# Optimization experiments

Measured on AMD Instinct MI355X. Metric: run time of the kernel, lower is better.

## Reference

```python
import jax, jax.numpy as jnp
import numpy as np

B, N = 32, 512


def _stick_breaking(b, x_mask):
    """Row-major stick-breaking recurrence, O(N^2) sequential steps.

    Equivalent to the TF while_loop: for step in range(N*N), m=step//N, n=step%N:
      fut      = max(0, x_mask[:,m,n+1:] - sum_{m'<m} x[:,m',n+1:])  (col partial sums)
      mfm      = sum_j fut_j
      row_sum  = sum_{n'<n} x[:,m,n']
      col_sum  = sum_{m'<m} x[:,m',n]
      lower    = mask[m,n]*max(0, 1 - row_sum - mfm)
      upper    = mask[m,n]*min(1 - row_sum, 1 - col_sum)
      x[m,n]   = lower + b[m,n]*(upper - lower)
    Key insight: during row m the column partial sums are constant, so the
    future-mass terms for every n can be precomputed as an exclusive reverse
    cumsum; only the within-row dependency (row_sum) needs a scan.
    """
    Bb, Nn, _ = b.shape
    dt = b.dtype

    def row_step(col_sums, inputs):
        b_row, mask_row = inputs                      # [B, N] each
        fut = jnp.maximum(0.0, mask_row - col_sums)   # [B, N]
        # mfm[:, n] = sum_{j > n} fut[:, j]  (exclusive reverse cumsum)
        mfm = jnp.flip(jnp.cumsum(jnp.flip(fut, -1), axis=-1), -1) - fut

        def col_step(row_sum, inp):
            b_mn, m_mn, mfm_n, cs_n = inp             # [B] each
            lower = m_mn * jnp.maximum(0.0, 1.0 - row_sum - mfm_n)
            upper = m_mn * jnp.minimum(1.0 - row_sum, 1.0 - cs_n)
            p = lower + b_mn * (upper - lower)
            return row_sum + p, p

        _, row = jax.lax.scan(
            col_step,
            jnp.zeros((Bb,), dt),
            (b_row.T, mask_row.T, mfm.T, col_sums.T),
        )
        row = row.T                                   # [B, N]
        return col_sums + row, row

    _, rows = jax.lax.scan(
        row_step,
        jnp.zeros((Bb, Nn), dt),
        (jnp.swapaxes(b, 0, 1), jnp.swapaxes(x_mask, 0, 1)),
    )
    return jnp.swapaxes(rows, 0, 1)                   # [B, N, N]


def setup_inputs() -> dict:
    key = jax.random.key(0)
    k1, _ = jax.random.split(key)
    x = jax.random.normal(k1, (B, N, N), dtype=jnp.float32)
    x_mask = jnp.ones((B, N, N), dtype=jnp.float32)
    return {"x": x, "x_mask": x_mask}


def reference(x, x_mask):
    # layer.call applies sigmoid to the logits before stick-breaking
    return _stick_breaking(jax.nn.sigmoid(x), x_mask)
```

## Files before the change

### kernel.cpp

```cpp
#include <hip/hip_runtime.h>

#define NBATCH 32
#define NDIM 512
#define NFAST 448
#define NPAIR 224
#define NWAVE 8


template <int CTRL, int RMASK>
__device__ __forceinline__ float dpp_add(float x) {
  int t = __builtin_amdgcn_update_dpp(0, __float_as_int(x), CTRL, RMASK, 0xf,
                                      false);
  return x + __int_as_float(t);
}

__device__ __forceinline__ float prefix_inc(float x) {
  x = dpp_add<0x111, 0xf>(x);
  x = dpp_add<0x112, 0xf>(x);
  x = dpp_add<0x114, 0xf>(x);
  x = dpp_add<0x118, 0xf>(x);
  x = dpp_add<0x142, 0xa>(x);
  x = dpp_add<0x143, 0xc>(x);
  return x;
}

__device__ __forceinline__ float wave_shr1(float x, float fill) {
  return __int_as_float(__builtin_amdgcn_update_dpp(
      __float_as_int(fill), __float_as_int(x), 0x138 , 0xf, 0xf,
      false));
}

template <int CTRL, int RMASK>
__device__ __forceinline__ void aff_step(float& A, float& B) {
  float Ae = __int_as_float(__builtin_amdgcn_update_dpp(
      __float_as_int(1.0f), __float_as_int(A), CTRL, RMASK, 0xf, false));
  float Be = __int_as_float(__builtin_amdgcn_update_dpp(
      0, __float_as_int(B), CTRL, RMASK, 0xf, false));
  B = fmaf(A, Be, B);
  A = A * Ae;
}

__device__ __forceinline__ void wg_barrier() {
  asm volatile("s_waitcnt lgkmcnt(0)" ::: "memory");
  __builtin_amdgcn_s_barrier();
  asm volatile("" ::: "memory");
}

__global__ __launch_bounds__(512, 2)
void sb_kernel(const float* __restrict__ x, const float* __restrict__ xm,
               float* __restrict__ out) {
  const int tid = (int)threadIdx.x;
  const int lane = tid & 63;
  const int w = __builtin_amdgcn_readfirstlane(tid >> 6);
  const size_t base =
      (size_t)blockIdx.x * NDIM * NDIM + (size_t)(w * 64 + lane);
  const float* xb = x + base;
  const float* mb = xm + base;
  float* ob = out + base;

  __shared__ float4 recs[NFAST];
  __shared__ alignas(16) float ex_sa[NWAVE];
  __shared__ alignas(16) float ex_S[NWAVE];
  __shared__ alignas(16) float ex_A[NWAVE];
  __shared__ alignas(16) float ex_B[NWAVE];

  float w8, t8;
  float c2_0, oc2_0, c2_1, oc2_1;
  float c1, c2, oc2;
  float fu = 0.0f, S = 0.0f;

  float X0 = xb[0], M0 = mb[0];
  float X1 = xb[NDIM], M1 = mb[NDIM];
  float p1x0 = xb[2 * NDIM], p1x1 = xb[3 * NDIM];
  float p1m0 = mb[2 * NDIM], p1m1 = mb[3 * NDIM];
  float p2x0 = xb[4 * NDIM], p2x1 = xb[5 * NDIM];
  float p2m0 = mb[4 * NDIM], p2m1 = mb[5 * NDIM];

  float Ax0, Ax1, Am0, Am1;
  float Bx0, Bx1, Bm0, Bm1;
  float Cx0, Cx1, Cm0, Cm1;
  Ax0 = Bx0 = Cx0 = p1x0;
  Ax1 = Bx1 = Cx1 = p1x1;
  Am0 = Bm0 = Cm0 = p1m0;
  Am1 = Bm1 = Cm1 = p1m1;
  switch (w % 3) {
    case 0:
      Bx0 = p1x0; Bx1 = p1x1; Bm0 = p1m0; Bm1 = p1m1;
      Cx0 = p2x0; Cx1 = p2x1; Cm0 = p2m0; Cm1 = p2m1;
      break;
    case 1:
      Cx0 = p1x0; Cx1 = p1x1; Cm0 = p1m0; Cm1 = p1m1;
      Ax0 = p2x0; Ax1 = p2x1; Am0 = p2m0; Am1 = p2m1;
      break;
    default:
      Ax0 = p1x0; Ax1 = p1x1; Am0 = p1m0; Am1 = p1m1;
      Bx0 = p2x0; Bx1 = p2x1; Bm0 = p2m0; Bm1 = p2m1;
      break;
  }

  {
    float sg0 = __builtin_amdgcn_rcpf(1.0f + __expf(-X0));
    c2_0 = M0 * sg0;
    oc2_0 = 1.0f - c2_0;
    float sg1 = __builtin_amdgcn_rcpf(1.0f + __expf(-X1));
    c2_1 = M1 * sg1;
    oc2_1 = 1.0f - c2_1;
    w8 = 1.0f;
    t8 = c2_0;
  }

  const float* px = xb + (long)(6 - 2 * w) * NDIM;
  const float* pm = mb + (long)(6 - 2 * w) * NDIM;
  float* po = ob - (long)(2 * w) * NDIM;

  auto row_fast = [&](int m, const float4& r, float c2r, float oc2r,
                      float* pO) {
    float PA = prefix_inc(t8);
    float uin = fmaxf(1.0f - (r.z + (PA - t8)), 0.0f);
    bool pW = w8 < uin;
    float A = pW ? 1.0f : oc2r;
    float Bv = pW ? (-t8) : 0.0f;
    aff_step<0x111, 0xf>(A, Bv);
    aff_step<0x112, 0xf>(A, Bv);
    aff_step<0x114, 0xf>(A, Bv);
    aff_step<0x118, 0xf>(A, Bv);
    aff_step<0x142, 0xa>(A, Bv);
    aff_step<0x143, 0xc>(A, Bv);
    float Aex = wave_shr1(A, 1.0f);
    float Bex = wave_shr1(Bv, 0.0f);
    if (w < NWAVE - 1 && lane == 63)
      recs[m] = make_float4(A * r.x, fmaf(A, r.y, Bv), r.z + PA, 0.0f);
    float E = r.x + r.y;
    float e = fminf(fmaxf(fmaf(Aex, E, Bex), 0.0f), 1.0f);
    float p = c2r * fminf(e, w8);
    w8 -= p;
    *pO = p;
  };

  auto pair_step = [&](int t, int k, float& WX0, float& WX1, float& WM0,
                       float& WM1, const float& RX0, const float& RX1,
                       const float& RM0, const float& RM1) {
    const int s = t - w;
    if ((unsigned)s < (unsigned)NPAIR) {
      const int m = 2 * s;
      float4 r0 = make_float4(1.0f, 0.0f, 0.0f, 0.0f), r1 = r0;
      if (w > 0) {
        r0 = recs[m];
        r1 = recs[m + 1];
      }
      const float* pxk = px + (size_t)(2 * k) * NDIM;
      const float* pmk = pm + (size_t)(2 * k) * NDIM;
      float LX0 = pxk[0], LX1 = pxk[NDIM];
      float LM0 = pmk[0], LM1 = pmk[NDIM];

      float sg0 = __builtin_amdgcn_rcpf(1.0f + __expf(-RX0));
      float c2n0 = RM0 * sg0;
      float oc2n0 = 1.0f - c2n0;
      float sg1 = __builtin_amdgcn_rcpf(1.0f + __expf(-RX1));
      float c2n1 = RM1 * sg1;
      float oc2n1 = 1.0f - c2n1;

      float* pok = po + (size_t)(2 * k) * NDIM;
      row_fast(m, r0, c2_0, oc2_0, pok);
      t8 = c2_1 * w8;
      row_fast(m + 1, r1, c2_1, oc2_1, pok + NDIM);
      t8 = c2n0 * w8;
      c2_0 = c2n0;
      oc2_0 = oc2n0;
      c2_1 = c2n1;
      oc2_1 = oc2n1;
      WX0 = LX0;
      WX1 = LX1;
      WM0 = LM0;
      WM1 = LM1;
    }
    wg_barrier();
  };

#pragma unroll 1
  for (int t = 0; t < NPAIR + NWAVE - 1; t += 3) {
    pair_step(t + 0, 0, Ax0, Ax1, Am0, Am1, Bx0, Bx1, Bm0, Bm1);
    pair_step(t + 1, 1, Bx0, Bx1, Bm0, Bm1, Cx0, Cx1, Cm0, Cm1);
    pair_step(t + 2, 2, Cx0, Cx1, Cm0, Cm1, Ax0, Ax1, Am0, Am1);
    px += 6 * NDIM;
    pm += 6 * NDIM;
    po += 6 * NDIM;
  }

  float fx0, fm0, fx1, fm1, fx2, fm2, fx3, fm3;
  {
    float m448 = mb[(size_t)448 * NDIM];
    fx1 = xb[(size_t)449 * NDIM];
    fm1 = mb[(size_t)449 * NDIM];
    fx2 = xb[(size_t)450 * NDIM];
    fm2 = mb[(size_t)450 * NDIM];
    fx3 = xb[(size_t)451 * NDIM];
    fm3 = mb[(size_t)451 * NDIM];
    fx0 = fx1;
    fm0 = fm1;
    c2 = c2_0;
    oc2 = oc2_0;
    c1 = m448 - c2;
    float om = 1.0f - m448;
    fu = fmaxf(w8 - om, 0.0f);
    S = fu;
  }

  auto row_full = [&](int m, float& WX, float& WM, const float& RX,
                      const float& RM) {
    const size_t nro = (size_t)((m + 4) & (NDIM - 1)) * NDIM;
    WX = xb[nro];
    WM = mb[nro];

    float PS = prefix_inc(S);
    float PA = prefix_inc(t8);

    if (lane == 63) {
      ex_sa[w] = PA;
      ex_S[w] = PS;
    }
    wg_barrier();

    float4 sl = *(const float4*)&ex_sa[0];
    float4 sh = *(const float4*)&ex_sa[4];
    float4 Sl = *(const float4*)&ex_S[0];
    float4 Sh = *(const float4*)&ex_S[4];
    float off_sa = 0.0f, off_S = 0.0f;
    if (w > 0) { off_sa += sl.x; off_S += Sl.x; }
    if (w > 1) { off_sa += sl.y; off_S += Sl.y; }
    if (w > 2) { off_sa += sl.z; off_S += Sl.z; }
    if (w > 3) { off_sa += sl.w; off_S += Sl.w; }
    if (w > 4) { off_sa += sh.x; off_S += Sh.x; }
    if (w > 5) { off_sa += sh.y; off_S += Sh.y; }
    if (w > 6) { off_sa += sh.z; off_S += Sh.z; }
    float Tg =
        ((Sl.x + Sl.y) + (Sl.z + Sl.w)) + ((Sh.x + Sh.y) + (Sh.z + Sh.w));

    float uin = fmaxf(1.0f - (off_sa + (PA - t8)), 0.0f);
    float R_ = (Tg - off_S) - PS;
    float nc1m = -c1 * R_;

    bool pW = w8 < uin;
    float aP = pW ? 1.0f : oc2;
    float bP = pW ? (-t8) : 0.0f;
    bool pL = (uin - R_) > 0.0f;
    if (pL) {
      aP -= c1;
      bP -= nc1m;
    }

    float A = aP, Bv = bP;
    aff_step<0x111, 0xf>(A, Bv);
    aff_step<0x112, 0xf>(A, Bv);
    aff_step<0x114, 0xf>(A, Bv);
    aff_step<0x118, 0xf>(A, Bv);
    aff_step<0x142, 0xa>(A, Bv);
    aff_step<0x143, 0xc>(A, Bv);
    float Aex = wave_shr1(A, 1.0f);
    float Bex = wave_shr1(Bv, 0.0f);

    if (lane == 63) {
      ex_A[w] = A;
      ex_B[w] = Bv;
    }
    wg_barrier();

    float4 Al = *(const float4*)&ex_A[0];
    float4 Ah = *(const float4*)&ex_A[4];
    float4 Bl = *(const float4*)&ex_B[0];
    float4 Bh = *(const float4*)&ex_B[4];
    float E = 1.0f;
    if (w > 0) E = fmaf(Al.x, E, Bl.x);
    if (w > 1) E = fmaf(Al.y, E, Bl.y);
    if (w > 2) E = fmaf(Al.z, E, Bl.z);
    if (w > 3) E = fmaf(Al.w, E, Bl.w);
    if (w > 4) E = fmaf(Ah.x, E, Bh.x);
    if (w > 5) E = fmaf(Ah.y, E, Bh.y);
    if (w > 6) E = fmaf(Ah.z, E, Bh.z);
    float e = fminf(fmaxf(fmaf(Aex, E, Bex), 0.0f), 1.0f);

    float sg = __builtin_amdgcn_rcpf(1.0f + __expf(-RX));
    float c2n = RM * sg;
    float oc2n = 1.0f - c2n;
    float c1n = RM - c2n;
    float omn = 1.0f - RM;

    float U = fminf(e, w8);
    float g = fmaxf(fmaf(c1, e, nc1m), 0.0f);
    float p = fmaf(c2, U, g);
    w8 -= p;
    ob[(size_t)m * NDIM] = p;

    t8 = c2n * w8;
    fu = fmaxf(w8 - omn, 0.0f);
    S = fu;
    c2 = c2n;
    oc2 = oc2n;
    c1 = c1n;
  };

#pragma unroll 1
  for (int m = NFAST; m < NDIM; m += 4) {
    row_full(m + 0, fx0, fm0, fx1, fm1);
    row_full(m + 1, fx1, fm1, fx2, fm2);
    row_full(m + 2, fx2, fm2, fx3, fm3);
    row_full(m + 3, fx3, fm3, fx0, fm0);
  }
}

extern "C" void kernel_launch(void* const* d_in, const int* in_sizes, int n_in,
                              void* d_out, int out_size, void* d_ws,
                              size_t ws_size, hipStream_t stream) {
  const float* x = (const float*)d_in[0];
  const float* xmask = (const float*)d_in[1];
  float* out = (float*)d_out;
  (void)in_sizes;
  (void)n_in;
  (void)out_size;
  (void)d_ws;
  (void)ws_size;
  hipLaunchKernelGGL(sb_kernel, dim3(NBATCH), dim3(512), 0, stream, x, xmask,
                     out);
}
```

Measured before the change: 271.6 us.

## Barrier once per three row-pairs with wavefront skew of three steps

Moves the workgroup barrier out of each pair step so it runs once per three-step group, and skews each wave by three pair-steps instead of one. Each wave is now aligned to the start of a group, which also removes the per-wave register rotation switch for the prefetched inputs. The aim is to cut barrier count roughly threefold. The cost is a longer pipeline fill and drain, since the loop now runs for 3*(NWAVE-1) extra steps, and waves may idle more at the edges.

```diff
diff --git a/kernel.cpp b/kernel.cpp
--- a/kernel.cpp
+++ b/kernel.cpp
@@ -52,6 +52,7 @@
   const int tid = (int)threadIdx.x;
   const int lane = tid & 63;
   const int w = __builtin_amdgcn_readfirstlane(tid >> 6);
+  const int w3 = 3 * w;
   const size_t base =
       (size_t)blockIdx.x * NDIM * NDIM + (size_t)(w * 64 + lane);
   const float* xb = x + base;
@@ -71,32 +72,11 @@
 
   float X0 = xb[0], M0 = mb[0];
   float X1 = xb[NDIM], M1 = mb[NDIM];
-  float p1x0 = xb[2 * NDIM], p1x1 = xb[3 * NDIM];
-  float p1m0 = mb[2 * NDIM], p1m1 = mb[3 * NDIM];
-  float p2x0 = xb[4 * NDIM], p2x1 = xb[5 * NDIM];
-  float p2m0 = mb[4 * NDIM], p2m1 = mb[5 * NDIM];
-
-  float Ax0, Ax1, Am0, Am1;
-  float Bx0, Bx1, Bm0, Bm1;
-  float Cx0, Cx1, Cm0, Cm1;
-  Ax0 = Bx0 = Cx0 = p1x0;
-  Ax1 = Bx1 = Cx1 = p1x1;
-  Am0 = Bm0 = Cm0 = p1m0;
-  Am1 = Bm1 = Cm1 = p1m1;
-  switch (w % 3) {
-    case 0:
-      Bx0 = p1x0; Bx1 = p1x1; Bm0 = p1m0; Bm1 = p1m1;
-      Cx0 = p2x0; Cx1 = p2x1; Cm0 = p2m0; Cm1 = p2m1;
-      break;
-    case 1:
-      Cx0 = p1x0; Cx1 = p1x1; Cm0 = p1m0; Cm1 = p1m1;
-      Ax0 = p2x0; Ax1 = p2x1; Am0 = p2m0; Am1 = p2m1;
-      break;
-    default:
-      Ax0 = p1x0; Ax1 = p1x1; Am0 = p1m0; Am1 = p1m1;
-      Bx0 = p2x0; Bx1 = p2x1; Bm0 = p2m0; Bm1 = p2m1;
-      break;
-  }
+  float Bx0 = xb[2 * NDIM], Bx1 = xb[3 * NDIM];
+  float Bm0 = mb[2 * NDIM], Bm1 = mb[3 * NDIM];
+  float Cx0 = xb[4 * NDIM], Cx1 = xb[5 * NDIM];
+  float Cm0 = mb[4 * NDIM], Cm1 = mb[5 * NDIM];
+  float Ax0 = Bx0, Ax1 = Bx1, Am0 = Bm0, Am1 = Bm1;
 
   {
     float sg0 = __builtin_amdgcn_rcpf(1.0f + __expf(-X0));
@@ -109,9 +89,9 @@
     t8 = c2_0;
   }
 
-  const float* px = xb + (long)(6 - 2 * w) * NDIM;
-  const float* pm = mb + (long)(6 - 2 * w) * NDIM;
-  float* po = ob - (long)(2 * w) * NDIM;
+  const float* px = xb + (long)(6 - 6 * w) * NDIM;
+  const float* pm = mb + (long)(6 - 6 * w) * NDIM;
+  float* po = ob - (long)(6 * w) * NDIM;
 
   auto row_fast = [&](int m, const float4& r, float c2r, float oc2r,
                       float* pO) {
@@ -140,7 +120,7 @@
   auto pair_step = [&](int t, int k, float& WX0, float& WX1, float& WM0,
                        float& WM1, const float& RX0, const float& RX1,
                        const float& RM0, const float& RM1) {
-    const int s = t - w;
+    const int s = t - w3;
     if ((unsigned)s < (unsigned)NPAIR) {
       const int m = 2 * s;
       float4 r0 = make_float4(1.0f, 0.0f, 0.0f, 0.0f), r1 = r0;
@@ -150,8 +130,10 @@
       }
       const float* pxk = px + (size_t)(2 * k) * NDIM;
       const float* pmk = pm + (size_t)(2 * k) * NDIM;
-      float LX0 = pxk[0], LX1 = pxk[NDIM];
-      float LM0 = pmk[0], LM1 = pmk[NDIM];
+      WX0 = pxk[0];
+      WX1 = pxk[NDIM];
+      WM0 = pmk[0];
+      WM1 = pmk[NDIM];
 
       float sg0 = __builtin_amdgcn_rcpf(1.0f + __expf(-RX0));
       float c2n0 = RM0 * sg0;
@@ -169,19 +151,15 @@
       oc2_0 = oc2n0;
       c2_1 = c2n1;
       oc2_1 = oc2n1;
-      WX0 = LX0;
-      WX1 = LX1;
-      WM0 = LM0;
-      WM1 = LM1;
     }
-    wg_barrier();
   };
 
 #pragma unroll 1
-  for (int t = 0; t < NPAIR + NWAVE - 1; t += 3) {
+  for (int t = 0; t < NPAIR + 3 * (NWAVE - 1); t += 3) {
     pair_step(t + 0, 0, Ax0, Ax1, Am0, Am1, Bx0, Bx1, Bm0, Bm1);
     pair_step(t + 1, 1, Bx0, Bx1, Bm0, Bm1, Cx0, Cx1, Cm0, Cm1);
     pair_step(t + 2, 2, Cx0, Cx1, Cm0, Cm1, Ax0, Ax1, Am0, Am1);
+    wg_barrier();
     px += 6 * NDIM;
     pm += 6 * NDIM;
     po += 6 * NDIM;
```

Result: no change. 274.0 us (+0.9%).
